# Kernel tuning notes

Measured on AMD Instinct MI355X. Metric: run time of the kernel, lower is better.

The kernel has to match this reference:

```python
import jax, jax.numpy as jnp
import numpy as np

NUM_LEVELS = 16
LEVEL_DIM = 2
BASE_RES = 16
DESIRED_RES = 2048
HASHMAP_SIZE = 2 ** 19
MULTIRES = 6
N_POINTS = 1048576

_scale = np.exp2(np.log2(DESIRED_RES / BASE_RES) / (NUM_LEVELS - 1))
RESOLUTIONS = [int(np.ceil(BASE_RES * _scale ** l)) for l in range(NUM_LEVELS)]
PRIMES = np.array([1, 2654435761, 805459861], dtype=np.uint32)
CORNERS = np.array([[i, j, k] for i in (0, 1) for j in (0, 1) for k in (0, 1)], dtype=np.int32)  # [8,3]


def positional_embed(x):
    # NeRF embedding (include_input, log-sampled freqs 2^0..2^(M-1)) -> [N, 3 + 3*2*M] = [N,39]
    freqs = (2.0 ** jnp.arange(MULTIRES)).astype(x.dtype)        # [M]
    xb = x[:, None, :] * freqs[None, :, None]                    # [N, M, 3]
    emb = jnp.concatenate([jnp.sin(xb), jnp.cos(xb)], axis=-1)   # [N, M, 6]
    return jnp.concatenate([x, emb.reshape(x.shape[0], -1)], axis=-1)


def hash_encode(x, tables):
    # multiresolution hash-grid trilinear lookup; x in [0,1]^3 -> [N, NUM_LEVELS*LEVEL_DIM]
    corners = jnp.asarray(CORNERS)       # [8,3]
    primes = jnp.asarray(PRIMES)         # [3] uint32
    outs = []
    for l, R in enumerate(RESOLUTIONS):  # fixed 16 levels (structurally distinct)
        pos = x * (R - 1)                # [N,3]
        p0 = jnp.floor(pos)
        w = pos - p0                     # fractional part, [N,3]
        c = p0.astype(jnp.int32)[:, None, :] + corners[None]   # [N,8,3] corner coords
        c = jnp.clip(c, 0, R - 1)
        if (R ** 3) <= HASHMAP_SIZE:
            idx = c[..., 0] + R * c[..., 1] + R * R * c[..., 2]  # direct (dense) indexing
        else:
            cu = c.astype(jnp.uint32)
            h = (cu[..., 0] * primes[0]) ^ (cu[..., 1] * primes[1]) ^ (cu[..., 2] * primes[2])
            idx = (h & jnp.uint32(HASHMAP_SIZE - 1)).astype(jnp.int32)
        wc = jnp.where(corners[None].astype(bool), w[:, None, :], 1.0 - w[:, None, :])  # [N,8,3]
        wc = jnp.prod(wc, axis=-1)        # trilinear weights [N,8]
        feats = tables[l][idx]            # gather [N,8,LEVEL_DIM]
        outs.append(jnp.sum(wc[..., None] * feats, axis=1))
    return jnp.concatenate(outs, axis=-1)


def softplus100(x):
    # torch.nn.Softplus(beta=100) with default threshold=20 (linear when beta*x > 20)
    return jnp.where(x * 100.0 > 20.0, x, jax.nn.softplus(x * 100.0) / 100.0)


def setup_inputs() -> dict:
    key = jax.random.key(0)
    ks = jax.random.split(key, 8)
    D_IN = 3 + 3 * 2 * MULTIRES + NUM_LEVELS * LEVEL_DIM  # 71
    x = jax.random.uniform(ks[0], (N_POINTS, 3), dtype=jnp.float32)
    tables = jax.random.uniform(ks[1], (NUM_LEVELS, HASHMAP_SIZE, LEVEL_DIM), minval=-1e-4, maxval=1e-4, dtype=jnp.float32)
    W0 = jax.random.normal(ks[2], (64, D_IN), dtype=jnp.float32) * (np.sqrt(2.0) / np.sqrt(64.0))
    b0 = jnp.zeros((64,), jnp.float32)
    W1 = jax.random.normal(ks[3], (64, 64), dtype=jnp.float32) * (np.sqrt(2.0) / np.sqrt(64.0))
    b1 = jnp.zeros((64,), jnp.float32)
    W2 = jnp.full((17, 64), np.sqrt(np.pi) / np.sqrt(64.0), jnp.float32) + jax.random.normal(ks[4], (17, 64), dtype=jnp.float32) * 1e-4
    b2 = jnp.full((17,), -1.0, jnp.float32)  # geometric init bias
    return {"x": x, "tables": tables, "W0": W0, "b0": b0, "W1": W1, "b1": b1, "W2": W2, "b2": b2}


def reference(x, tables, W0, b0, W1, b1, W2, b2):
    # divide_factor = 1.0 -> encoding sees x directly
    feat = hash_encode(x, tables)                                   # [N,32]
    h = jnp.concatenate([positional_embed(x), feat], axis=-1)       # [N,71]
    h = softplus100(h @ W0.T + b0)                                  # [N,64]
    h = softplus100(h @ W1.T + b1)                                  # [N,64]
    return h @ W2.T + b2                                            # [N,17] = (sdf, 16 features)
```

## Files before the change

### kernel.cpp

```cpp
#include <hip/hip_runtime.h>
#include <stdint.h>

#define HMAP   (1u << 19)
#define HMASK  (HMAP - 1u)

typedef short bf16x8 __attribute__((ext_vector_type(8)));
typedef float f32x4  __attribute__((ext_vector_type(4)));

__device__ __constant__ const int c_res[16] = {16, 23, 31, 43, 59, 81, 112, 154, 213, 295, 407, 562, 777, 1073, 1483, 2048};

__device__ __forceinline__ unsigned short f2bf(float f) {
    unsigned u = __float_as_uint(f);
    u += 0x7fffu + ((u >> 16) & 1u);
    return (unsigned short)(u >> 16);
}

__device__ __forceinline__ float softplus100(float v) {
    return fmaxf(v, 0.f) + 0.01f * __logf(1.f + __expf(-100.f * fabsf(v)));
}

__device__ __forceinline__ bf16x8 cvt8(const float* __restrict__ p) {
    f32x4 a = *(const f32x4*)p;
    f32x4 b = *(const f32x4*)(p + 4);
    bf16x8 r;
    r[0] = f2bf(a[0]); r[1] = f2bf(a[1]); r[2] = f2bf(a[2]); r[3] = f2bf(a[3]);
    r[4] = f2bf(b[0]); r[5] = f2bf(b[1]); r[6] = f2bf(b[2]); r[7] = f2bf(b[3]);
    return r;
}

__device__ __forceinline__ float2 gather_level(const float* __restrict__ tab, int R,
                                               float x0, float x1, float x2) {
    const float Rm1 = (float)(R - 1);
    float px = x0 * Rm1, py = x1 * Rm1, pz = x2 * Rm1;
    float fx = floorf(px), fy = floorf(py), fz = floorf(pz);
    float wx = px - fx, wy = py - fy, wz = pz - fz;
    int ix = (int)fx, iy = (int)fy, iz = (int)fz;
    ix = max(0, min(ix, R - 1)); iy = max(0, min(iy, R - 1)); iz = max(0, min(iz, R - 1));
    int jx = min(ix + 1, R - 1), jy = min(iy + 1, R - 1), jz = min(iz + 1, R - 1);
    float ax = 1.f - wx, ay = 1.f - wy, az = 1.f - wz;
    float wyz0 = ay * az, wyz1 = wy * az, wyz2 = ay * wz, wyz3 = wy * wz;
    float2 lo[4], hi[4];
    const bool adj = (jx == ix + 1);
    if ((long long)R * R * R <= (long long)HMAP) {
        unsigned sy = (unsigned)R, sz = (unsigned)(R * R);
        unsigned base0 = (unsigned)iy * sy + (unsigned)iz * sz;
        unsigned base1 = (unsigned)jy * sy + (unsigned)iz * sz;
        unsigned base2 = (unsigned)iy * sy + (unsigned)jz * sz;
        unsigned base3 = (unsigned)jy * sy + (unsigned)jz * sz;
        unsigned bases[4] = {base0, base1, base2, base3};
        const float2* t2 = (const float2*)tab;
        #pragma unroll
        for (int k = 0; k < 4; ++k) {
            unsigned i0 = bases[k] + (unsigned)ix;
            if (adj && !(i0 & 1u)) {
                f32x4 q = *(const f32x4*)(tab + ((size_t)i0 << 1));
                lo[k] = make_float2(q[0], q[1]);
                hi[k] = make_float2(q[2], q[3]);
            } else {
                lo[k] = t2[i0];
                hi[k] = t2[bases[k] + (unsigned)jx];
            }
        }
    } else {
        unsigned hy0 = (unsigned)iy * 2654435761u, hy1 = (unsigned)jy * 2654435761u;
        unsigned hz0 = (unsigned)iz * 805459861u,  hz1 = (unsigned)jz * 805459861u;
        unsigned m0 = hy0 ^ hz0, m1 = hy1 ^ hz0, m2 = hy0 ^ hz1, m3 = hy1 ^ hz1;
        unsigned ms[4] = {m0, m1, m2, m3};
        if (adj && ((ix & 1) == 0)) {
            #pragma unroll
            for (int k = 0; k < 4; ++k) {
                unsigned h = ((unsigned)ix ^ ms[k]) & HMASK;
                f32x4 q = *(const f32x4*)(tab + ((size_t)(h & ~1u) << 1));
                float2 e0 = make_float2(q[0], q[1]);
                float2 e1 = make_float2(q[2], q[3]);
                bool sw = (h & 1u) != 0;
                lo[k] = sw ? e1 : e0;
                hi[k] = sw ? e0 : e1;
            }
        } else {
            const float2* t2 = (const float2*)tab;
            #pragma unroll
            for (int k = 0; k < 4; ++k) {
                unsigned hl = ((unsigned)ix ^ ms[k]) & HMASK;
                unsigned hh = ((unsigned)jx ^ ms[k]) & HMASK;
                lo[k] = t2[hl];
                hi[k] = t2[hh];
            }
        }
    }
    float2 r = make_float2(0.f, 0.f);
    float wyz[4] = {wyz0, wyz1, wyz2, wyz3};
    #pragma unroll
    for (int k = 0; k < 4; ++k) {
        float wl = ax * wyz[k], wh = wx * wyz[k];
        r.x += wl * lo[k].x + wh * hi[k].x;
        r.y += wl * lo[k].y + wh * hi[k].y;
    }
    return r;
}

__global__ __launch_bounds__(256, 8)
void gather_levels(const float* __restrict__ x, const float* __restrict__ tables,
                   unsigned* __restrict__ feat, int N, int C) {
    const int b = blockIdx.x;
    const int half = 8 * C;
    int r, level;
    if (b < half) { r = b; level = r & 7; }
    else          { r = b - half; level = 15 - (r & 7); }
    const size_t p = (size_t)(r >> 3) * 256 + threadIdx.x;
    const float x0 = __builtin_nontemporal_load(x + 3 * p);
    const float x1 = __builtin_nontemporal_load(x + 3 * p + 1);
    const float x2 = __builtin_nontemporal_load(x + 3 * p + 2);
    float2 f = gather_level(tables + (size_t)level * (2u * HMAP), c_res[level], x0, x1, x2);
    unsigned v = (unsigned)f2bf(f.x) | ((unsigned)f2bf(f.y) << 16);
    __builtin_nontemporal_store(v, feat + (size_t)level * N + p);
}

#define NPB       128
#define TILES     8
#define PTS_BLK   (NPB * TILES)
#define SA_STRIDE 104
#define SW0_OFF   (128 * 104)
#define SMEM_SHORTS (SW0_OFF + 64 * 104)

__global__ __launch_bounds__(256, 4)
void mlp_tiled(const float* __restrict__ x, const unsigned* __restrict__ feat,
               const float* __restrict__ W0, const float* __restrict__ b0,
               const float* __restrict__ W1, const float* __restrict__ b1,
               const float* __restrict__ W2, const float* __restrict__ b2,
               float* __restrict__ out, int N) {
    __shared__ unsigned short smem[SMEM_SHORTS];
    const int tid  = threadIdx.x;
    const int blk  = blockIdx.x;
    const int wave = tid >> 6, lane = tid & 63;
    const int mhalf = (wave & 1) * 64;
    const int nhalf = (wave >> 1);
    const int lrow = lane & 15, quad = lane >> 4;

    for (int i = tid; i < 64 * 104; i += 256) {
        int n = i / 104, k = i - n * 104;
        smem[SW0_OFF + i] = (k < 71) ? f2bf(W0[n * 71 + k]) : (unsigned short)0;
    }
    for (int i = tid; i < 128 * 25; i += 256) {
        int p = i / 25, k = i - p * 25;
        smem[p * SA_STRIDE + 71 + k] = 0;
    }
    bf16x8 w1f[2][2];
    #pragma unroll
    for (int ks = 0; ks < 2; ++ks)
        #pragma unroll
        for (int nt = 0; nt < 2; ++nt) {
            int n = nhalf * 32 + nt * 16 + lrow;
            w1f[ks][nt] = cvt8(W1 + n * 64 + ks * 32 + quad * 8);
        }
    bf16x8 w2f[2];
    {
        int n2 = nhalf * 16 + lrow;
        #pragma unroll
        for (int ks = 0; ks < 2; ++ks) {
            if (n2 < 17) w2f[ks] = cvt8(W2 + n2 * 64 + ks * 32 + quad * 8);
            else { bf16x8 z = {0,0,0,0,0,0,0,0}; w2f[ks] = z; }
        }
    }
    float b0v[2], b1v[2], b2v;
    #pragma unroll
    for (int nt = 0; nt < 2; ++nt) {
        b0v[nt] = b0[nhalf * 32 + nt * 16 + lrow];
        b1v[nt] = b1[nhalf * 32 + nt * 16 + lrow];
    }
    { int c2 = nhalf * 16 + lrow; b2v = (c2 < 17) ? b2[c2] : 0.f; }
    __syncthreads();

    const size_t pbase0 = (size_t)blk * PTS_BLK;
    #pragma unroll 1
    for (int t = 0; t < TILES; ++t) {
        const size_t pb = pbase0 + (size_t)t * NPB;
        {
            const int p = tid & 127;
            const size_t gp = pb + p;
            unsigned short* row = &smem[p * SA_STRIDE];
            const float x0 = __builtin_nontemporal_load(x + 3 * gp);
            const float x1 = __builtin_nontemporal_load(x + 3 * gp + 1);
            const float x2 = __builtin_nontemporal_load(x + 3 * gp + 2);
            if (tid < 128) {
                row[0] = f2bf(x0); row[1] = f2bf(x1); row[2] = f2bf(x2);
                float fr = 1.f;
                #pragma unroll
                for (int m = 0; m < 6; ++m) {
                    row[3 + 6 * m + 0] = f2bf(__sinf(x0 * fr));
                    row[3 + 6 * m + 1] = f2bf(__sinf(x1 * fr));
                    row[3 + 6 * m + 2] = f2bf(__sinf(x2 * fr));
                    fr *= 2.f;
                }
            } else {
                float fr = 1.f;
                #pragma unroll
                for (int m = 0; m < 6; ++m) {
                    row[3 + 6 * m + 3] = f2bf(__cosf(x0 * fr));
                    row[3 + 6 * m + 4] = f2bf(__cosf(x1 * fr));
                    row[3 + 6 * m + 5] = f2bf(__cosf(x2 * fr));
                    fr *= 2.f;
                }
                #pragma unroll
                for (int l = 0; l < 16; ++l) {
                    unsigned v = __builtin_nontemporal_load(feat + (size_t)l * N + gp);
                    row[39 + 2 * l] = (unsigned short)(v & 0xffffu);
                    row[40 + 2 * l] = (unsigned short)(v >> 16);
                }
            }
        }
        __syncthreads();

        f32x4 acc0[4][2];
        #pragma unroll
        for (int mt = 0; mt < 4; ++mt)
            #pragma unroll
            for (int nt = 0; nt < 2; ++nt) acc0[mt][nt] = (f32x4){0.f, 0.f, 0.f, 0.f};
        #pragma unroll
        for (int ks = 0; ks < 3; ++ks) {
            bf16x8 bfr[2];
            #pragma unroll
            for (int nt = 0; nt < 2; ++nt) {
                int n = nhalf * 32 + nt * 16 + lrow;
                bfr[nt] = *(const bf16x8*)&smem[SW0_OFF + n * 104 + ks * 32 + quad * 8];
            }
            #pragma unroll
            for (int mt = 0; mt < 4; ++mt) {
                int m = mhalf + mt * 16 + lrow;
                bf16x8 afr = *(const bf16x8*)&smem[m * SA_STRIDE + ks * 32 + quad * 8];
                #pragma unroll
                for (int nt = 0; nt < 2; ++nt)
                    acc0[mt][nt] = __builtin_amdgcn_mfma_f32_16x16x32_bf16(afr, bfr[nt], acc0[mt][nt], 0, 0, 0);
            }
        }
        __syncthreads();
        #pragma unroll
        for (int mt = 0; mt < 4; ++mt)
            #pragma unroll
            for (int nt = 0; nt < 2; ++nt) {
                int colg = nhalf * 32 + nt * 16 + lrow;
                #pragma unroll
                for (int r = 0; r < 4; ++r) {
                    int rowm = mhalf + mt * 16 + quad * 4 + r;
                    smem[rowm * SA_STRIDE + colg] = f2bf(softplus100(acc0[mt][nt][r] + b0v[nt]));
                }
            }
        __syncthreads();

        f32x4 acc1[4][2];
        #pragma unroll
        for (int mt = 0; mt < 4; ++mt)
            #pragma unroll
            for (int nt = 0; nt < 2; ++nt) acc1[mt][nt] = (f32x4){0.f, 0.f, 0.f, 0.f};
        #pragma unroll
        for (int ks = 0; ks < 2; ++ks) {
            #pragma unroll
            for (int mt = 0; mt < 4; ++mt) {
                int m = mhalf + mt * 16 + lrow;
                bf16x8 afr = *(const bf16x8*)&smem[m * SA_STRIDE + ks * 32 + quad * 8];
                #pragma unroll
                for (int nt = 0; nt < 2; ++nt)
                    acc1[mt][nt] = __builtin_amdgcn_mfma_f32_16x16x32_bf16(afr, w1f[ks][nt], acc1[mt][nt], 0, 0, 0);
            }
        }
        __syncthreads();
        #pragma unroll
        for (int mt = 0; mt < 4; ++mt)
            #pragma unroll
            for (int nt = 0; nt < 2; ++nt) {
                int colg = nhalf * 32 + nt * 16 + lrow;
                #pragma unroll
                for (int r = 0; r < 4; ++r) {
                    int rowm = mhalf + mt * 16 + quad * 4 + r;
                    smem[rowm * SA_STRIDE + colg] = f2bf(softplus100(acc1[mt][nt][r] + b1v[nt]));
                }
            }
        __syncthreads();

        f32x4 acc2[4];
        #pragma unroll
        for (int mt = 0; mt < 4; ++mt) acc2[mt] = (f32x4){0.f, 0.f, 0.f, 0.f};
        #pragma unroll
        for (int ks = 0; ks < 2; ++ks) {
            #pragma unroll
            for (int mt = 0; mt < 4; ++mt) {
                int m = mhalf + mt * 16 + lrow;
                bf16x8 afr = *(const bf16x8*)&smem[m * SA_STRIDE + ks * 32 + quad * 8];
                acc2[mt] = __builtin_amdgcn_mfma_f32_16x16x32_bf16(afr, w2f[ks], acc2[mt], 0, 0, 0);
            }
        }
        {
            int colg = nhalf * 16 + lrow;
            if (colg < 17) {
                #pragma unroll
                for (int mt = 0; mt < 4; ++mt)
                    #pragma unroll
                    for (int r = 0; r < 4; ++r) {
                        int rowm = mhalf + mt * 16 + quad * 4 + r;
                        __builtin_nontemporal_store(acc2[mt][r] + b2v,
                                                    out + (pb + rowm) * 17 + colg);
                    }
            }
        }
        __syncthreads();
    }
}

__global__ __launch_bounds__(256, 3)
void gn_fused(const float* __restrict__ x, const float* __restrict__ tables,
              const float* __restrict__ W0, const float* __restrict__ b0,
              const float* __restrict__ W1, const float* __restrict__ b1,
              const float* __restrict__ W2, const float* __restrict__ b2,
              float* __restrict__ out) {
    __shared__ unsigned short smem[SMEM_SHORTS];
    const int tid = threadIdx.x;
    const int blk = blockIdx.x;
    const int wave = tid >> 6, lane = tid & 63;
    const int mhalf = (wave & 1) * 64;
    const int nhalf = (wave >> 1);
    const int lrow = lane & 15, quad = lane >> 4;
    for (int i = tid; i < 64 * 104; i += 256) {
        int n = i / 104, k = i - n * 104;
        smem[SW0_OFF + i] = (k < 71) ? f2bf(W0[n * 71 + k]) : (unsigned short)0;
    }
    for (int i = tid; i < 128 * 25; i += 256) {
        int p = i / 25, k = i - p * 25;
        smem[p * SA_STRIDE + 71 + k] = 0;
    }
    bf16x8 w1f[2][2];
    #pragma unroll
    for (int ks = 0; ks < 2; ++ks)
        #pragma unroll
        for (int nt = 0; nt < 2; ++nt) {
            int n = nhalf * 32 + nt * 16 + lrow;
            w1f[ks][nt] = cvt8(W1 + n * 64 + ks * 32 + quad * 8);
        }
    bf16x8 w2f[2];
    {
        int n2 = nhalf * 16 + lrow;
        #pragma unroll
        for (int ks = 0; ks < 2; ++ks) {
            if (n2 < 17) w2f[ks] = cvt8(W2 + n2 * 64 + ks * 32 + quad * 8);
            else { bf16x8 z = {0,0,0,0,0,0,0,0}; w2f[ks] = z; }
        }
    }
    float b0v[2], b1v[2], b2v;
    #pragma unroll
    for (int nt = 0; nt < 2; ++nt) {
        b0v[nt] = b0[nhalf * 32 + nt * 16 + lrow];
        b1v[nt] = b1[nhalf * 32 + nt * 16 + lrow];
    }
    { int c2 = nhalf * 16 + lrow; b2v = (c2 < 17) ? b2[c2] : 0.f; }
    {
        const int p = tid & 127;
        const size_t gp = (size_t)blk * NPB + p;
        const float x0 = x[3 * gp], x1 = x[3 * gp + 1], x2 = x[3 * gp + 2];
        unsigned short* row = &smem[p * SA_STRIDE];
        if (tid < 128) {
            row[0] = f2bf(x0); row[1] = f2bf(x1); row[2] = f2bf(x2);
            float fr = 1.f;
            #pragma unroll
            for (int m = 0; m < 6; ++m) {
                row[3 + 6 * m + 0] = f2bf(__sinf(x0 * fr));
                row[3 + 6 * m + 1] = f2bf(__sinf(x1 * fr));
                row[3 + 6 * m + 2] = f2bf(__sinf(x2 * fr));
                fr *= 2.f;
            }
            #pragma unroll
            for (int li = 0; li < 8; ++li) {
                const int l = 2 * li;
                float2 f = gather_level(tables + (size_t)l * (2u * HMAP), c_res[l], x0, x1, x2);
                row[39 + 2 * l] = f2bf(f.x);
                row[40 + 2 * l] = f2bf(f.y);
            }
        } else {
            float fr = 1.f;
            #pragma unroll
            for (int m = 0; m < 6; ++m) {
                row[3 + 6 * m + 3] = f2bf(__cosf(x0 * fr));
                row[3 + 6 * m + 4] = f2bf(__cosf(x1 * fr));
                row[3 + 6 * m + 5] = f2bf(__cosf(x2 * fr));
                fr *= 2.f;
            }
            #pragma unroll
            for (int li = 0; li < 8; ++li) {
                const int l = 2 * li + 1;
                float2 f = gather_level(tables + (size_t)l * (2u * HMAP), c_res[l], x0, x1, x2);
                row[39 + 2 * l] = f2bf(f.x);
                row[40 + 2 * l] = f2bf(f.y);
            }
        }
    }
    __syncthreads();
    f32x4 acc0[4][2];
    #pragma unroll
    for (int mt = 0; mt < 4; ++mt)
        #pragma unroll
        for (int nt = 0; nt < 2; ++nt) acc0[mt][nt] = (f32x4){0.f, 0.f, 0.f, 0.f};
    #pragma unroll
    for (int ks = 0; ks < 3; ++ks) {
        bf16x8 bfr[2];
        #pragma unroll
        for (int nt = 0; nt < 2; ++nt) {
            int n = nhalf * 32 + nt * 16 + lrow;
            bfr[nt] = *(const bf16x8*)&smem[SW0_OFF + n * 104 + ks * 32 + quad * 8];
        }
        #pragma unroll
        for (int mt = 0; mt < 4; ++mt) {
            int m = mhalf + mt * 16 + lrow;
            bf16x8 afr = *(const bf16x8*)&smem[m * SA_STRIDE + ks * 32 + quad * 8];
            #pragma unroll
            for (int nt = 0; nt < 2; ++nt)
                acc0[mt][nt] = __builtin_amdgcn_mfma_f32_16x16x32_bf16(afr, bfr[nt], acc0[mt][nt], 0, 0, 0);
        }
    }
    __syncthreads();
    #pragma unroll
    for (int mt = 0; mt < 4; ++mt)
        #pragma unroll
        for (int nt = 0; nt < 2; ++nt) {
            int colg = nhalf * 32 + nt * 16 + lrow;
            #pragma unroll
            for (int r = 0; r < 4; ++r) {
                int rowm = mhalf + mt * 16 + quad * 4 + r;
                smem[rowm * SA_STRIDE + colg] = f2bf(softplus100(acc0[mt][nt][r] + b0v[nt]));
            }
        }
    __syncthreads();
    f32x4 acc1[4][2];
    #pragma unroll
    for (int mt = 0; mt < 4; ++mt)
        #pragma unroll
        for (int nt = 0; nt < 2; ++nt) acc1[mt][nt] = (f32x4){0.f, 0.f, 0.f, 0.f};
    #pragma unroll
    for (int ks = 0; ks < 2; ++ks) {
        #pragma unroll
        for (int mt = 0; mt < 4; ++mt) {
            int m = mhalf + mt * 16 + lrow;
            bf16x8 afr = *(const bf16x8*)&smem[m * SA_STRIDE + ks * 32 + quad * 8];
            #pragma unroll
            for (int nt = 0; nt < 2; ++nt)
                acc1[mt][nt] = __builtin_amdgcn_mfma_f32_16x16x32_bf16(afr, w1f[ks][nt], acc1[mt][nt], 0, 0, 0);
        }
    }
    __syncthreads();
    #pragma unroll
    for (int mt = 0; mt < 4; ++mt)
        #pragma unroll
        for (int nt = 0; nt < 2; ++nt) {
            int colg = nhalf * 32 + nt * 16 + lrow;
            #pragma unroll
            for (int r = 0; r < 4; ++r) {
                int rowm = mhalf + mt * 16 + quad * 4 + r;
                smem[rowm * SA_STRIDE + colg] = f2bf(softplus100(acc1[mt][nt][r] + b1v[nt]));
            }
        }
    __syncthreads();
    f32x4 acc2[4];
    #pragma unroll
    for (int mt = 0; mt < 4; ++mt) acc2[mt] = (f32x4){0.f, 0.f, 0.f, 0.f};
    #pragma unroll
    for (int ks = 0; ks < 2; ++ks) {
        #pragma unroll
        for (int mt = 0; mt < 4; ++mt) {
            int m = mhalf + mt * 16 + lrow;
            bf16x8 afr = *(const bf16x8*)&smem[m * SA_STRIDE + ks * 32 + quad * 8];
            acc2[mt] = __builtin_amdgcn_mfma_f32_16x16x32_bf16(afr, w2f[ks], acc2[mt], 0, 0, 0);
        }
    }
    {
        int colg = nhalf * 16 + lrow;
        if (colg < 17) {
            #pragma unroll
            for (int mt = 0; mt < 4; ++mt)
                #pragma unroll
                for (int r = 0; r < 4; ++r) {
                    int rowm = mhalf + mt * 16 + quad * 4 + r;
                    out[((size_t)blk * NPB + rowm) * 17 + colg] = acc2[mt][r] + b2v;
                }
        }
    }
}

extern "C" void kernel_launch(void* const* d_in, const int* in_sizes, int n_in,
                              void* d_out, int out_size, void* d_ws, size_t ws_size,
                              hipStream_t stream) {
    const float* x      = (const float*)d_in[0];
    const float* tables = (const float*)d_in[1];
    const float* W0     = (const float*)d_in[2];
    const float* b0     = (const float*)d_in[3];
    const float* W1     = (const float*)d_in[4];
    const float* b1     = (const float*)d_in[5];
    const float* W2     = (const float*)d_in[6];
    const float* b2     = (const float*)d_in[7];
    float* out = (float*)d_out;
    const int n = in_sizes[0] / 3;
    const size_t ws_needed = (size_t)16 * n * 4;
    if (ws_size >= ws_needed) {
        unsigned* feat = (unsigned*)d_ws;
        const int C = n / 256;
        gather_levels<<<dim3(16 * C), dim3(256), 0, stream>>>(x, tables, feat, n, C);
        mlp_tiled<<<dim3(n / PTS_BLK), dim3(256), 0, stream>>>(x, feat, W0, b0, W1, b1, W2, b2, out, n);
    } else {
        gn_fused<<<dim3(n / NPB), dim3(256), 0, stream>>>(x, tables, W0, b0, W1, b1, W2, b2, out);
    }
}
```

Measured before the change: 594.7 us.

## Fuse hash-grid gather into tiled MLP kernel, drop workspace feature buffer

Replaces the two-kernel path (a level-major gather kernel writing bf16 features to workspace, then a tiled MLP kernel) with one persistent-tile kernel that performs the hash-grid lookups inline before each MLP tile, and halves tiles per block. This removes the feature round-trip through global memory and one launch. In exchange it gives up the level-major scheduling that kept one level's table hot in cache across blocks, so the random table gathers may hit L2/MALL less and the MLP stalls on gather latency.

New measurement: 958.4 us. 1.61x slower.

```diff
diff --git a/kernel.cpp b/kernel.cpp
--- a/kernel.cpp
+++ b/kernel.cpp
@@ -99,36 +99,19 @@
     return r;
 }
 
-__global__ __launch_bounds__(256, 8)
-void gather_levels(const float* __restrict__ x, const float* __restrict__ tables,
-                   unsigned* __restrict__ feat, int N, int C) {
-    const int b = blockIdx.x;
-    const int half = 8 * C;
-    int r, level;
-    if (b < half) { r = b; level = r & 7; }
-    else          { r = b - half; level = 15 - (r & 7); }
-    const size_t p = (size_t)(r >> 3) * 256 + threadIdx.x;
-    const float x0 = __builtin_nontemporal_load(x + 3 * p);
-    const float x1 = __builtin_nontemporal_load(x + 3 * p + 1);
-    const float x2 = __builtin_nontemporal_load(x + 3 * p + 2);
-    float2 f = gather_level(tables + (size_t)level * (2u * HMAP), c_res[level], x0, x1, x2);
-    unsigned v = (unsigned)f2bf(f.x) | ((unsigned)f2bf(f.y) << 16);
-    __builtin_nontemporal_store(v, feat + (size_t)level * N + p);
-}
-
 #define NPB       128
-#define TILES     8
+#define TILES     4
 #define PTS_BLK   (NPB * TILES)
 #define SA_STRIDE 104
 #define SW0_OFF   (128 * 104)
 #define SMEM_SHORTS (SW0_OFF + 64 * 104)
 
 __global__ __launch_bounds__(256, 4)
-void mlp_tiled(const float* __restrict__ x, const unsigned* __restrict__ feat,
-               const float* __restrict__ W0, const float* __restrict__ b0,
-               const float* __restrict__ W1, const float* __restrict__ b1,
-               const float* __restrict__ W2, const float* __restrict__ b2,
-               float* __restrict__ out, int N) {
+void fused_tiled(const float* __restrict__ x, const float* __restrict__ tables,
+                 const float* __restrict__ W0, const float* __restrict__ b0,
+                 const float* __restrict__ W1, const float* __restrict__ b1,
+                 const float* __restrict__ W2, const float* __restrict__ b2,
+                 float* __restrict__ out) {
     __shared__ unsigned short smem[SMEM_SHORTS];
     const int tid  = threadIdx.x;
     const int blk  = blockIdx.x;
@@ -179,9 +162,9 @@
             const int p = tid & 127;
             const size_t gp = pb + p;
             unsigned short* row = &smem[p * SA_STRIDE];
-            const float x0 = __builtin_nontemporal_load(x + 3 * gp);
-            const float x1 = __builtin_nontemporal_load(x + 3 * gp + 1);
-            const float x2 = __builtin_nontemporal_load(x + 3 * gp + 2);
+            const float x0 = x[3 * gp];
+            const float x1 = x[3 * gp + 1];
+            const float x2 = x[3 * gp + 2];
             if (tid < 128) {
                 row[0] = f2bf(x0); row[1] = f2bf(x1); row[2] = f2bf(x2);
                 float fr = 1.f;
@@ -192,6 +175,13 @@
                     row[3 + 6 * m + 2] = f2bf(__sinf(x2 * fr));
                     fr *= 2.f;
                 }
+                #pragma unroll
+                for (int li = 0; li < 8; ++li) {
+                    const int l = 2 * li;
+                    float2 f = gather_level(tables + (size_t)l * (2u * HMAP), c_res[l], x0, x1, x2);
+                    row[39 + 2 * l] = f2bf(f.x);
+                    row[40 + 2 * l] = f2bf(f.y);
+                }
             } else {
                 float fr = 1.f;
                 #pragma unroll
@@ -202,10 +192,11 @@
                     fr *= 2.f;
                 }
                 #pragma unroll
-                for (int l = 0; l < 16; ++l) {
-                    unsigned v = __builtin_nontemporal_load(feat + (size_t)l * N + gp);
-                    row[39 + 2 * l] = (unsigned short)(v & 0xffffu);
-                    row[40 + 2 * l] = (unsigned short)(v >> 16);
+                for (int li = 0; li < 8; ++li) {
+                    const int l = 2 * li + 1;
+                    float2 f = gather_level(tables + (size_t)l * (2u * HMAP), c_res[l], x0, x1, x2);
+                    row[39 + 2 * l] = f2bf(f.x);
+                    row[40 + 2 * l] = f2bf(f.y);
                 }
             }
         }
@@ -303,182 +294,6 @@
             }
         }
         __syncthreads();
-    }
-}
-
-__global__ __launch_bounds__(256, 3)
-void gn_fused(const float* __restrict__ x, const float* __restrict__ tables,
-              const float* __restrict__ W0, const float* __restrict__ b0,
-              const float* __restrict__ W1, const float* __restrict__ b1,
-              const float* __restrict__ W2, const float* __restrict__ b2,
-              float* __restrict__ out) {
-    __shared__ unsigned short smem[SMEM_SHORTS];
-    const int tid = threadIdx.x;
-    const int blk = blockIdx.x;
-    const int wave = tid >> 6, lane = tid & 63;
-    const int mhalf = (wave & 1) * 64;
-    const int nhalf = (wave >> 1);
-    const int lrow = lane & 15, quad = lane >> 4;
-    for (int i = tid; i < 64 * 104; i += 256) {
-        int n = i / 104, k = i - n * 104;
-        smem[SW0_OFF + i] = (k < 71) ? f2bf(W0[n * 71 + k]) : (unsigned short)0;
-    }
-    for (int i = tid; i < 128 * 25; i += 256) {
-        int p = i / 25, k = i - p * 25;
-        smem[p * SA_STRIDE + 71 + k] = 0;
-    }
-    bf16x8 w1f[2][2];
-    #pragma unroll
-    for (int ks = 0; ks < 2; ++ks)
-        #pragma unroll
-        for (int nt = 0; nt < 2; ++nt) {
-            int n = nhalf * 32 + nt * 16 + lrow;
-            w1f[ks][nt] = cvt8(W1 + n * 64 + ks * 32 + quad * 8);
-        }
-    bf16x8 w2f[2];
-    {
-        int n2 = nhalf * 16 + lrow;
-        #pragma unroll
-        for (int ks = 0; ks < 2; ++ks) {
-            if (n2 < 17) w2f[ks] = cvt8(W2 + n2 * 64 + ks * 32 + quad * 8);
-            else { bf16x8 z = {0,0,0,0,0,0,0,0}; w2f[ks] = z; }
-        }
-    }
-    float b0v[2], b1v[2], b2v;
-    #pragma unroll
-    for (int nt = 0; nt < 2; ++nt) {
-        b0v[nt] = b0[nhalf * 32 + nt * 16 + lrow];
-        b1v[nt] = b1[nhalf * 32 + nt * 16 + lrow];
-    }
-    { int c2 = nhalf * 16 + lrow; b2v = (c2 < 17) ? b2[c2] : 0.f; }
-    {
-        const int p = tid & 127;
-        const size_t gp = (size_t)blk * NPB + p;
-        const float x0 = x[3 * gp], x1 = x[3 * gp + 1], x2 = x[3 * gp + 2];
-        unsigned short* row = &smem[p * SA_STRIDE];
-        if (tid < 128) {
-            row[0] = f2bf(x0); row[1] = f2bf(x1); row[2] = f2bf(x2);
-            float fr = 1.f;
-            #pragma unroll
-            for (int m = 0; m < 6; ++m) {
-                row[3 + 6 * m + 0] = f2bf(__sinf(x0 * fr));
-                row[3 + 6 * m + 1] = f2bf(__sinf(x1 * fr));
-                row[3 + 6 * m + 2] = f2bf(__sinf(x2 * fr));
-                fr *= 2.f;
-            }
-            #pragma unroll
-            for (int li = 0; li < 8; ++li) {
-                const int l = 2 * li;
-                float2 f = gather_level(tables + (size_t)l * (2u * HMAP), c_res[l], x0, x1, x2);
-                row[39 + 2 * l] = f2bf(f.x);
-                row[40 + 2 * l] = f2bf(f.y);
-            }
-        } else {
-            float fr = 1.f;
-            #pragma unroll
-            for (int m = 0; m < 6; ++m) {
-                row[3 + 6 * m + 3] = f2bf(__cosf(x0 * fr));
-                row[3 + 6 * m + 4] = f2bf(__cosf(x1 * fr));
-                row[3 + 6 * m + 5] = f2bf(__cosf(x2 * fr));
-                fr *= 2.f;
-            }
-            #pragma unroll
-            for (int li = 0; li < 8; ++li) {
-                const int l = 2 * li + 1;
-                float2 f = gather_level(tables + (size_t)l * (2u * HMAP), c_res[l], x0, x1, x2);
-                row[39 + 2 * l] = f2bf(f.x);
-                row[40 + 2 * l] = f2bf(f.y);
-            }
-        }
-    }
-    __syncthreads();
-    f32x4 acc0[4][2];
-    #pragma unroll
-    for (int mt = 0; mt < 4; ++mt)
-        #pragma unroll
-        for (int nt = 0; nt < 2; ++nt) acc0[mt][nt] = (f32x4){0.f, 0.f, 0.f, 0.f};
-    #pragma unroll
-    for (int ks = 0; ks < 3; ++ks) {
-        bf16x8 bfr[2];
-        #pragma unroll
-        for (int nt = 0; nt < 2; ++nt) {
-            int n = nhalf * 32 + nt * 16 + lrow;
-            bfr[nt] = *(const bf16x8*)&smem[SW0_OFF + n * 104 + ks * 32 + quad * 8];
-        }
-        #pragma unroll
-        for (int mt = 0; mt < 4; ++mt) {
-            int m = mhalf + mt * 16 + lrow;
-            bf16x8 afr = *(const bf16x8*)&smem[m * SA_STRIDE + ks * 32 + quad * 8];
-            #pragma unroll
-            for (int nt = 0; nt < 2; ++nt)
-                acc0[mt][nt] = __builtin_amdgcn_mfma_f32_16x16x32_bf16(afr, bfr[nt], acc0[mt][nt], 0, 0, 0);
-        }
-    }
-    __syncthreads();
-    #pragma unroll
-    for (int mt = 0; mt < 4; ++mt)
-        #pragma unroll
-        for (int nt = 0; nt < 2; ++nt) {
-            int colg = nhalf * 32 + nt * 16 + lrow;
-            #pragma unroll
-            for (int r = 0; r < 4; ++r) {
-                int rowm = mhalf + mt * 16 + quad * 4 + r;
-                smem[rowm * SA_STRIDE + colg] = f2bf(softplus100(acc0[mt][nt][r] + b0v[nt]));
-            }
-        }
-    __syncthreads();
-    f32x4 acc1[4][2];
-    #pragma unroll
-    for (int mt = 0; mt < 4; ++mt)
-        #pragma unroll
-        for (int nt = 0; nt < 2; ++nt) acc1[mt][nt] = (f32x4){0.f, 0.f, 0.f, 0.f};
-    #pragma unroll
-    for (int ks = 0; ks < 2; ++ks) {
-        #pragma unroll
-        for (int mt = 0; mt < 4; ++mt) {
-            int m = mhalf + mt * 16 + lrow;
-            bf16x8 afr = *(const bf16x8*)&smem[m * SA_STRIDE + ks * 32 + quad * 8];
-            #pragma unroll
-            for (int nt = 0; nt < 2; ++nt)
-                acc1[mt][nt] = __builtin_amdgcn_mfma_f32_16x16x32_bf16(afr, w1f[ks][nt], acc1[mt][nt], 0, 0, 0);
-        }
-    }
-    __syncthreads();
-    #pragma unroll
-    for (int mt = 0; mt < 4; ++mt)
-        #pragma unroll
-        for (int nt = 0; nt < 2; ++nt) {
-            int colg = nhalf * 32 + nt * 16 + lrow;
-            #pragma unroll
-            for (int r = 0; r < 4; ++r) {
-                int rowm = mhalf + mt * 16 + quad * 4 + r;
-                smem[rowm * SA_STRIDE + colg] = f2bf(softplus100(acc1[mt][nt][r] + b1v[nt]));
-            }
-        }
-    __syncthreads();
-    f32x4 acc2[4];
-    #pragma unroll
-    for (int mt = 0; mt < 4; ++mt) acc2[mt] = (f32x4){0.f, 0.f, 0.f, 0.f};
-    #pragma unroll
-    for (int ks = 0; ks < 2; ++ks) {
-        #pragma unroll
-        for (int mt = 0; mt < 4; ++mt) {
-            int m = mhalf + mt * 16 + lrow;
-            bf16x8 afr = *(const bf16x8*)&smem[m * SA_STRIDE + ks * 32 + quad * 8];
-            acc2[mt] = __builtin_amdgcn_mfma_f32_16x16x32_bf16(afr, w2f[ks], acc2[mt], 0, 0, 0);
-        }
-    }
-    {
-        int colg = nhalf * 16 + lrow;
-        if (colg < 17) {
-            #pragma unroll
-            for (int mt = 0; mt < 4; ++mt)
-                #pragma unroll
-                for (int r = 0; r < 4; ++r) {
-                    int rowm = mhalf + mt * 16 + quad * 4 + r;
-                    out[((size_t)blk * NPB + rowm) * 17 + colg] = acc2[mt][r] + b2v;
-                }
-        }
     }
 }
 
@@ -495,13 +310,5 @@
     const float* b2     = (const float*)d_in[7];
     float* out = (float*)d_out;
     const int n = in_sizes[0] / 3;
-    const size_t ws_needed = (size_t)16 * n * 4;
-    if (ws_size >= ws_needed) {
-        unsigned* feat = (unsigned*)d_ws;
-        const int C = n / 256;
-        gather_levels<<<dim3(16 * C), dim3(256), 0, stream>>>(x, tables, feat, n, C);
-        mlp_tiled<<<dim3(n / PTS_BLK), dim3(256), 0, stream>>>(x, feat, W0, b0, W1, b1, W2, b2, out, n);
-    } else {
-        gn_fused<<<dim3(n / NPB), dim3(256), 0, stream>>>(x, tables, W0, b0, W1, b1, W2, b2, out);
-    }
-}
+    fused_tiled<<<dim3(n / PTS_BLK), dim3(256), 0, stream>>>(x, tables, W0, b0, W1, b1, W2, b2, out);
+}
```
